# Kernel optimization log

Measured on AMD Instinct MI355X. Metric: run time of the kernel, lower is better.

The kernel has to match this reference:

```python
import jax, jax.numpy as jnp
import numpy as np

S = 8            # n_internal_streams
N = 2**S - 1     # 255 cliques (all non-empty subsets of streams)
D = 32           # half_dim = consciousness_dim // 2
INPUT_DIM = 512
NUM_ITER = 5
B = 1024


def _configs():
    # binary membership of each clique (non-empty subsets), [N, S]
    return ((np.arange(1, 2**S)[:, None] >> np.arange(S)) & 1).astype(np.float32)


def setup_inputs() -> dict:
    key = jax.random.key(0)
    ks = jax.random.split(key, 10)
    cfg = _configs()
    depths = cfg.sum(-1)
    # topological amplitude init: gaussian profile over clique depth
    center, sigma = S / 2.0, S / 3.0
    prof = np.exp(-((depths - center) ** 2) / (2 * sigma ** 2))
    prof = prof / (np.linalg.norm(prof) + 1e-8)
    psi_A0 = jnp.asarray(np.broadcast_to(prof[None, :, None], (1, N, D)).copy(),
                         jnp.float32) + jax.random.normal(ks[0], (1, N, D)) * 0.01
    inp = {
        'network_state': jax.random.normal(ks[1], (B, INPUT_DIM), jnp.float32),
        'W_streams': jax.random.normal(ks[2], (S * D, INPUT_DIM)) / np.sqrt(INPUT_DIM),
        'b_streams': jnp.zeros((S * D,), jnp.float32),
        'W_A': jax.random.normal(ks[3], (D, D)) / np.sqrt(D),
        'b_A': jnp.zeros((D,), jnp.float32),
        'W_phi': jax.random.normal(ks[4], (D, D)) / np.sqrt(D),
        'b_phi': jnp.zeros((D,), jnp.float32),
        'psi_A0': psi_A0,
        'psi_phi0': jax.random.normal(ks[5], (1, N, D)) * 0.3,
        'W_comp': jax.random.normal(ks[6], (32, N)) / np.sqrt(N),
        'b_comp': jnp.zeros((32,), jnp.float32),
        'W_read': jax.random.normal(ks[7], (2 * D, 32 * D)) / np.sqrt(32 * D),
        'b_read': jnp.zeros((2 * D,), jnp.float32),
        'alpha_kin': jnp.asarray(0.5, jnp.float32),
        'mass_sq': jnp.asarray(0.1, jnp.float32),
        'potential_weight': jnp.asarray(0.3, jnp.float32),
        'input_weight': jnp.asarray(0.5, jnp.float32),
        'evolution_rate': jnp.asarray(0.3, jnp.float32),
        'phase_coupling': jnp.asarray(1.0, jnp.float32),
    }
    return inp


def reference(network_state, W_streams, b_streams, W_A, b_A, W_phi, b_phi,
              psi_A0, psi_phi0, W_comp, b_comp, W_read, b_read,
              alpha_kin, mass_sq, potential_weight, input_weight,
              evolution_rate, phase_coupling):
    cfg = jnp.asarray(_configs())                      # [N,S]
    depths = cfg.sum(-1)                               # [N]
    # Hamming-distance kernel between clique configurations
    Ham = cfg @ (1.0 - cfg).T + (1.0 - cfg) @ cfg.T    # [N,N]
    K = jnp.exp(-Ham / S)
    krow = K.sum(1)                                    # [N]

    Bb = network_state.shape[0]
    feats = (network_state @ W_streams.T + b_streams).reshape(Bb, S, D)
    # clique features: mean of member-stream features
    cf = jnp.einsum('ns,bsd->bnd', cfg, feats) / depths[None, :, None]
    A_input = jax.nn.softplus(cf @ W_A.T + b_A)        # [B,N,D]
    phi_input = jnp.pi * jnp.tanh(cf @ W_phi.T + b_phi)

    A = jax.nn.softplus(jnp.broadcast_to(psi_A0, (Bb, N, D)))
    phi = jnp.broadcast_to(psi_phi0, (Bb, N, D))
    dt = jax.nn.sigmoid(evolution_rate)

    for _ in range(NUM_ITER):
        # laplacian: sum_j K_ij (A_j - A_i) / N  (factorized, same math)
        KA = jnp.einsum('ij,bjd->bid', K, A)
        lap = (KA - krow[None, :, None] * A) / N
        sp, cp = jnp.sin(phi), jnp.cos(phi)
        Ks = jnp.einsum('ij,bjd->bid', K, sp)
        Kc = jnp.einsum('ij,bjd->bid', K, cp)
        # sum_j K_ij A_i sin(phi_j - phi_i) / N
        pc = A * (cp * Ks - sp * Kc) / N
        # nonlocal potential: V_i = sum_j K_ij A_j cos(phi_j - phi_i) / N
        KAc = jnp.einsum('ij,bjd->bid', K, A * cp)
        KAs = jnp.einsum('ij,bjd->bid', K, A * sp)
        V = (cp * KAc + sp * KAs) / N
        input_drive = A_input * jnp.sin(phi_input - phi)
        dA = (alpha_kin * lap + potential_weight * V - mass_sq * A
              + input_weight * (A_input - A))
        A = jax.nn.softplus(A + dt * dA)               # updated A used in dphi
        dphi = alpha_kin * pc / (A + 1e-8) + input_weight * input_drive
        phi = phi + dt * dphi
        # per-clique norm clip to 1
        norms = jnp.maximum(jnp.linalg.norm(A, axis=-1, keepdims=True), 1e-8)
        A = A * jnp.where(norms > 1.0, 1.0 / norms, 1.0)

    A_t = jnp.swapaxes(A, 1, 2)                        # [B,D,N]
    Ac = jax.nn.relu(A_t @ W_comp.T + b_comp)          # [B,D,32]
    ro = Ac.reshape(Bb, -1) @ W_read.T + b_read        # [B,2D]
    amplitude = jax.nn.softplus(ro[:, :D])
    phase = jnp.tanh(ro[:, D:] * phase_coupling) * jnp.pi
    psi = (amplitude * jnp.cos(phase)).astype(jnp.complex64) + 1j * (amplitude * jnp.sin(phase)).astype(jnp.complex64)
    return psi, amplitude, phase
```

## Files before the change

kernel.cpp:

```cpp
#include <hip/hip_runtime.h>
#include <math.h>

#define PI_F   3.14159265358979f
#define QF     0.88249690258459546f
#define INV255 (1.0f/255.0f)

__device__ __forceinline__ float softplus_f(float x){
    return fmaxf(x, 0.0f) + __logf(1.0f + __expf(-fabsf(x)));
}
__device__ __forceinline__ float tanh_fast(float x){
    const float e = __expf(2.0f*x);
    return fmaf(-2.0f, __builtin_amdgcn_rcpf(e + 1.0f), 1.0f);
}

template<int CTRL>
__device__ __forceinline__ float dppmov(float x){
    return __int_as_float(__builtin_amdgcn_mov_dpp(__float_as_int(x), CTRL, 0xF, 0xF, false));
}
__device__ __forceinline__ float lxor1 (float x){ return dppmov<0xB1>(x);  }
__device__ __forceinline__ float lxor2 (float x){ return dppmov<0x4E>(x);  }
__device__ __forceinline__ float lxor8 (float x){ return dppmov<0x128>(x); }
__device__ __forceinline__ float lxor4 (float x){ return __int_as_float(__builtin_amdgcn_ds_swizzle(__float_as_int(x), 0x101F)); }
__device__ __forceinline__ float lxor16(float x){ return __int_as_float(__builtin_amdgcn_ds_swizzle(__float_as_int(x), 0x401F)); }
__device__ __forceinline__ float lxor32(float x){ return __shfl_xor(x, 32, 64); }

template<int CTRL>
__device__ __forceinline__ float dppadd(float v){
    return v + __int_as_float(__builtin_amdgcn_update_dpp(0, __float_as_int(v), CTRL, 0xF, 0xF, true));
}
__device__ __forceinline__ float wave_sum63(float v){
    v = dppadd<0x111>(v);
    v = dppadd<0x112>(v);
    v = dppadd<0x114>(v);
    v = dppadd<0x118>(v);
    v = dppadd<0x142>(v);
    v = dppadd<0x143>(v);
    return v;
}

template<int NA>
__device__ __forceinline__ void bflyN(float (&x)[NA][4]){
    const float qv = QF;
    #pragma unroll
    for (int a = 0; a < NA; a++){
        #pragma unroll
        for (int r = 0; r < 4; r++) x[a][r] = fmaf(lxor1 (x[a][r]), qv, x[a][r]);
    }
    #pragma unroll
    for (int a = 0; a < NA; a++){
        #pragma unroll
        for (int r = 0; r < 4; r++) x[a][r] = fmaf(lxor2 (x[a][r]), qv, x[a][r]);
    }
    #pragma unroll
    for (int a = 0; a < NA; a++){
        #pragma unroll
        for (int r = 0; r < 4; r++) x[a][r] = fmaf(lxor8 (x[a][r]), qv, x[a][r]);
    }
    #pragma unroll
    for (int a = 0; a < NA; a++){
        #pragma unroll
        for (int r = 0; r < 4; r++) x[a][r] = fmaf(lxor4 (x[a][r]), qv, x[a][r]);
    }
    #pragma unroll
    for (int a = 0; a < NA; a++){
        #pragma unroll
        for (int r = 0; r < 4; r++) x[a][r] = fmaf(lxor16(x[a][r]), qv, x[a][r]);
    }
    #pragma unroll
    for (int a = 0; a < NA; a++){
        #pragma unroll
        for (int r = 0; r < 4; r++) x[a][r] = fmaf(lxor32(x[a][r]), qv, x[a][r]);
    }
    #pragma unroll
    for (int a = 0; a < NA; a++){
        float t0 = x[a][0], t2 = x[a][2];
        x[a][0] = fmaf(QF, x[a][1], x[a][0]);
        x[a][1] = fmaf(QF, t0,      x[a][1]);
        x[a][2] = fmaf(QF, x[a][3], x[a][2]);
        x[a][3] = fmaf(QF, t2,      x[a][3]);
        t0 = x[a][0]; float t1 = x[a][1];
        x[a][0] = fmaf(QF, x[a][2], x[a][0]);
        x[a][1] = fmaf(QF, x[a][3], x[a][1]);
        x[a][2] = fmaf(QF, t0,      x[a][2]);
        x[a][3] = fmaf(QF, t1,      x[a][3]);
    }
}

__global__ __launch_bounds__(256) void prep_kernel(
        const float* __restrict__ Ws,    const float* __restrict__ psiA0,
        const float* __restrict__ psiP0, const float* __restrict__ p_alpha,
        const float* __restrict__ p_msq, const float* __restrict__ p_pw,
        const float* __restrict__ p_iw,  const float* __restrict__ p_evo,
        float* __restrict__ WsT,  float* __restrict__ Xc,  float* __restrict__ P0c,
        float* __restrict__ S0c,  float* __restrict__ C0c, float* __restrict__ F0c)
{
    if (blockIdx.x < 32){
        __shared__ float tile[64][65];
        const int rt = blockIdx.x & 3, ct = blockIdx.x >> 2;
        const int r0 = rt*64, c0t = ct*64;
        const int tx = threadIdx.x & 63, ty = threadIdx.x >> 6;
        #pragma unroll
        for (int k = 0; k < 16; k++){
            const int row = ty*16 + k;
            tile[row][tx] = Ws[(r0+row)*512 + c0t + tx];
        }
        __syncthreads();
        #pragma unroll
        for (int k = 0; k < 16; k++){
            const int row = ty*16 + k;
            WsT[(c0t+row)*256 + r0 + tx] = tile[tx][row];
        }
        return;
    }
    const int tid = threadIdx.x;
    const int w = tid >> 6, l = tid & 63;
    const float alpha = p_alpha[0], msq = p_msq[0], pw = p_pw[0], iw = p_iw[0];
    const float dt   = 1.0f / (1.0f + __expf(-p_evo[0]));
    const float dta  = dt * alpha * INV255;
    const float dtpw = dt * pw * INV255;
    const float c0   = 1.0f - dt * (msq + iw);
    const float m0 = (l == 0) ? 0.0f : 1.0f;
    int nn[4]; float krow[4];
    float c18;
    { const float t1 = 1.0f + QF, t2 = t1*t1, t4 = t2*t2; c18 = t4*t4; }
    #pragma unroll
    for (int r = 0; r < 4; r++){
        nn[r] = l + 64*r;
        krow[r] = c18 - __expf(-0.125f * (float)__popc(nn[r]));
    }
    #pragma unroll
    for (int dd = 0; dd < 8; dd++){
        const int d = w*8 + dd;
        float A0[4], ph0[4], sp[4], cp[4];
        float x[5][4];
        #pragma unroll
        for (int r = 0; r < 4; r++){
            const int n = nn[r];
            A0[r]  = (n > 0) ? softplus_f(psiA0[(n-1)*32 + d]) : 0.0f;
            ph0[r] = (n > 0) ? psiP0[(n-1)*32 + d] : 0.0f;
            sp[r] = __sinf(ph0[r]); cp[r] = __cosf(ph0[r]);
            const float mk = (r == 0) ? m0 : 1.0f;
            const float xa = A0[r] * mk;
            x[0][r] = xa;
            x[1][r] = sp[r] * mk;
            x[2][r] = cp[r] * mk;
            x[3][r] = xa * cp[r];
            x[4][r] = xa * sp[r];
        }
        bflyN<5>(x);
        #pragma unroll
        for (int r = 0; r < 4; r++){
            const float Ao   = A0[r];
            const float lapp = fmaf(-krow[r], Ao, x[0][r]);
            const float Vp   = fmaf(cp[r], x[3][r], sp[r]*x[4][r]);
            const float Pp   = fmaf(-sp[r], x[2][r], cp[r]*x[1][r]);
            float X = c0 * Ao;
            X = fmaf(dta,  lapp, X);
            X = fmaf(dtpw, Vp,   X);
            const int idx = d*256 + nn[r];
            Xc[idx]  = X;
            P0c[idx] = dta * Ao * Pp;
            S0c[idx] = sp[r];
            C0c[idx] = cp[r];
            F0c[idx] = ph0[r];
        }
    }
}

template<bool USET>
__global__ __launch_bounds__(256) void fused_kernel(
        const float* __restrict__ ns,
        const float* __restrict__ Ws,
        const float* __restrict__ WsT,
        const float* __restrict__ bs,
        const float* __restrict__ WA,
        const float* __restrict__ bA,
        const float* __restrict__ WP,
        const float* __restrict__ bP,
        const float* __restrict__ psiA0,
        const float* __restrict__ psiP0,
        const float* __restrict__ Xc,
        const float* __restrict__ P0c,
        const float* __restrict__ S0c,
        const float* __restrict__ C0c,
        const float* __restrict__ F0c,
        const float* __restrict__ Wcomp,
        const float* __restrict__ bcomp,
        const float* __restrict__ Wread,
        const float* __restrict__ bread,
        const float* __restrict__ p_alpha, const float* __restrict__ p_msq,
        const float* __restrict__ p_pw,    const float* __restrict__ p_iw,
        const float* __restrict__ p_evo,   const float* __restrict__ p_pcpl,
        float* __restrict__ out, int Bb)
{
    __shared__ __align__(16) float nsb[512];
    __shared__ __align__(16) float fe[256];
    __shared__ __align__(16) float hA[256];
    __shared__ __align__(16) float hP[256];
    __shared__ __align__(16) float red[2][1024];
    __shared__ __align__(16) float ac[1024];
    __shared__ __align__(16) float rop[256];

    const int b   = blockIdx.x;
    const int tid = threadIdx.x;
    const int w   = tid >> 6, l = tid & 63;

    const float alpha = p_alpha[0], msq = p_msq[0], pw = p_pw[0], iw = p_iw[0];
    const float pcpl  = p_pcpl[0];
    const float dt    = 1.0f / (1.0f + __expf(-p_evo[0]));
    const float dta  = dt * alpha * INV255;
    const float dtpw = dt * pw * INV255;
    const float c0   = 1.0f - dt * (msq + iw);
    const float dtiw = dt * iw;

    nsb[tid]       = ns[b*512 + tid];
    nsb[tid + 256] = ns[b*512 + 256 + tid];
    __syncthreads();
    if (USET){
        float f = bs[tid];
        const float4* nb4 = (const float4*)nsb;
        #pragma unroll 8
        for (int j4 = 0; j4 < 128; j4++){
            const float4 nv = nb4[j4];
            const float* col = WsT + j4*1024 + tid;
            f = fmaf(col[0],   nv.x, f);
            f = fmaf(col[256], nv.y, f);
            f = fmaf(col[512], nv.z, f);
            f = fmaf(col[768], nv.w, f);
        }
        fe[tid] = f;
    } else {
        float f = bs[tid];
        const float4* wr  = (const float4*)(Ws + tid*512);
        const float4* nb4 = (const float4*)nsb;
        #pragma unroll 8
        for (int i = 0; i < 128; i++){
            const float4 wv = wr[i], nv = nb4[i];
            f = fmaf(wv.x, nv.x, f); f = fmaf(wv.y, nv.y, f);
            f = fmaf(wv.z, nv.z, f); f = fmaf(wv.w, nv.w, f);
        }
        fe[tid] = f;
    }
    __syncthreads();
    {
        const int s = tid >> 5, d = tid & 31;
        float a = 0.0f, p = 0.0f;
        #pragma unroll 8
        for (int dp = 0; dp < 32; dp++){
            const float fv = fe[s*32 + dp];
            a = fmaf(WA[d*32 + dp], fv, a);
            p = fmaf(WP[d*32 + dp], fv, p);
        }
        hA[tid] = a; hP[tid] = p;
    }
    __syncthreads();

    int   nn[4];
    float krow[4], rdep[4];
    const float m0 = (l == 0) ? 0.0f : 1.0f;
    float c18;
    { const float t1 = 1.0f + QF, t2 = t1*t1, t4 = t2*t2; c18 = t4*t4; }
    #pragma unroll
    for (int r = 0; r < 4; r++){
        nn[r] = l + 64*r;
        const int pop = __popc(nn[r]);
        krow[r]  = c18 - __expf(-0.125f * (float)pop);
        rdep[r]  = 1.0f / (float)(pop ? pop : 1);
    }

    float A[8][4], phi[8][4], CAp[8][4], Dsp[8][4], Dcp[8][4];
    float nrm0[4] = {0.f, 0.f, 0.f, 0.f};

    #pragma unroll
    for (int dd = 0; dd < 8; dd++){
        const int d = w*8 + dd;
        const float bAd = bA[d], bPd = bP[d];
        float gA_[8], gP_[8];
        #pragma unroll
        for (int s = 0; s < 8; s++){ gA_[s] = hA[s*32 + d]; gP_[s] = hP[s*32 + d]; }
        #pragma unroll
        for (int r = 0; r < 4; r++){
            float sA = 0.0f, sP = 0.0f;
            #pragma unroll
            for (int s = 0; s < 8; s++){
                if ((nn[r] >> s) & 1){ sA += gA_[s]; sP += gP_[s]; }
            }
            const float uA  = fmaf(sA, rdep[r], bAd);
            const float uP  = fmaf(sP, rdep[r], bPd);
            const float Ain = softplus_f(uA);
            const float pin = PI_F * tanh_fast(uP);
            const float si = __sinf(pin), ci = __cosf(pin);
            const float ca = dtiw * Ain;
            CAp[dd][r] = ca; Dsp[dd][r] = ca * si; Dcp[dd][r] = ca * ci;
            if (USET){
                const int idx = d*256 + nn[r];
                const float An = softplus_f(Xc[idx] + ca);
                const float rr = __builtin_amdgcn_rcpf(An + 1e-8f);
                float pb = fmaf(Dsp[dd][r], C0c[idx], F0c[idx]);
                pb = fmaf(-Dcp[dd][r], S0c[idx], pb);
                phi[dd][r] = fmaf(P0c[idx], rr, pb);
                A[dd][r]   = An;
                nrm0[r]    = fmaf(An, An, nrm0[r]);
            } else {
                const int nm1 = (nn[r] > 0) ? (nn[r] - 1) : 0;
                A[dd][r]   = softplus_f(psiA0[nm1*32 + d]);
                phi[dd][r] = psiP0[nm1*32 + d];
            }
        }
    }

    if (USET){
        #pragma unroll
        for (int r = 0; r < 4; r++) red[0][w*256 + nn[r]] = nrm0[r];
        __syncthreads();
        float scl[4];
        #pragma unroll
        for (int r = 0; r < 4; r++){
            const float t = red[0][nn[r]] + red[0][256 + nn[r]]
                          + red[0][512 + nn[r]] + red[0][768 + nn[r]];
            scl[r] = (t > 1.0f) ? rsqrtf(t) : 1.0f;
        }
        #pragma unroll
        for (int dd = 0; dd < 8; dd++)
            #pragma unroll
            for (int r = 0; r < 4; r++) A[dd][r] *= scl[r];
    }

    const int NFULL = USET ? 3 : 4;
    for (int it = 0; it < NFULL; it++){
        const int pbuf = USET ? ((it + 1) & 1) : (it & 1);
        float nrm[4] = {0.f, 0.f, 0.f, 0.f};
        #pragma unroll
        for (int dd = 0; dd < 8; dd++){
            float sp[4], cp[4];
            float x[5][4];
            {
                sp[0] = __sinf(phi[dd][0]); cp[0] = __cosf(phi[dd][0]);
                const float xa = A[dd][0] * m0;
                x[0][0] = xa;
                x[1][0] = sp[0] * m0;
                x[2][0] = cp[0] * m0;
                x[3][0] = xa * cp[0];
                x[4][0] = xa * sp[0];
            }
            #pragma unroll
            for (int r = 1; r < 4; r++){
                sp[r] = __sinf(phi[dd][r]); cp[r] = __cosf(phi[dd][r]);
                const float xa = A[dd][r];
                x[0][r] = xa;
                x[1][r] = sp[r];
                x[2][r] = cp[r];
                x[3][r] = xa * cp[r];
                x[4][r] = xa * sp[r];
            }
            bflyN<5>(x);
            #pragma unroll
            for (int r = 0; r < 4; r++){
                const float Ao   = A[dd][r];
                const float lapp = fmaf(-krow[r], Ao, x[0][r]);
                const float Vp   = fmaf(cp[r], x[3][r], sp[r]*x[4][r]);
                float Aarg = fmaf(c0, Ao, CAp[dd][r]);
                Aarg = fmaf(dta,  lapp, Aarg);
                Aarg = fmaf(dtpw, Vp,   Aarg);
                const float An = softplus_f(Aarg);
                const float Pp = fmaf(-sp[r], x[2][r], cp[r]*x[1][r]);
                const float rr = __builtin_amdgcn_rcpf(An + 1e-8f);
                float pb = fmaf(Dsp[dd][r], cp[r], phi[dd][r]);
                pb = fmaf(-Dcp[dd][r], sp[r], pb);
                phi[dd][r] = fmaf(dta*Ao, Pp*rr, pb);
                A[dd][r]   = An;
                nrm[r]     = fmaf(An, An, nrm[r]);
            }
        }
        #pragma unroll
        for (int r = 0; r < 4; r++) red[pbuf][w*256 + nn[r]] = nrm[r];
        __syncthreads();
        float scl[4];
        #pragma unroll
        for (int r = 0; r < 4; r++){
            const float t = red[pbuf][nn[r]] + red[pbuf][256 + nn[r]]
                          + red[pbuf][512 + nn[r]] + red[pbuf][768 + nn[r]];
            scl[r] = (t > 1.0f) ? rsqrtf(t) : 1.0f;
        }
        #pragma unroll
        for (int dd = 0; dd < 8; dd++)
            #pragma unroll
            for (int r = 0; r < 4; r++) A[dd][r] *= scl[r];
    }

    {
        float nrm[4] = {0.f, 0.f, 0.f, 0.f};
        #pragma unroll
        for (int dd = 0; dd < 8; dd++){
            float sp[4], cp[4];
            float y[3][4];
            {
                sp[0] = __sinf(phi[dd][0]); cp[0] = __cosf(phi[dd][0]);
                const float xa = A[dd][0] * m0;
                y[0][0] = xa;
                y[1][0] = xa * cp[0];
                y[2][0] = xa * sp[0];
            }
            #pragma unroll
            for (int r = 1; r < 4; r++){
                sp[r] = __sinf(phi[dd][r]); cp[r] = __cosf(phi[dd][r]);
                const float xa = A[dd][r];
                y[0][r] = xa;
                y[1][r] = xa * cp[r];
                y[2][r] = xa * sp[r];
            }
            bflyN<3>(y);
            #pragma unroll
            for (int r = 0; r < 4; r++){
                const float Ao   = A[dd][r];
                const float lapp = fmaf(-krow[r], Ao, y[0][r]);
                const float Vp   = fmaf(cp[r], y[1][r], sp[r]*y[2][r]);
                float Aarg = fmaf(c0, Ao, CAp[dd][r]);
                Aarg = fmaf(dta,  lapp, Aarg);
                Aarg = fmaf(dtpw, Vp,   Aarg);
                const float An = softplus_f(Aarg);
                A[dd][r]   = An;
                nrm[r]     = fmaf(An, An, nrm[r]);
            }
        }
        #pragma unroll
        for (int r = 0; r < 4; r++) red[0][w*256 + nn[r]] = nrm[r];
        __syncthreads();
        float scl[4];
        #pragma unroll
        for (int r = 0; r < 4; r++){
            const float t = red[0][nn[r]] + red[0][256 + nn[r]]
                          + red[0][512 + nn[r]] + red[0][768 + nn[r]];
            scl[r] = (t > 1.0f) ? rsqrtf(t) : 1.0f;
        }
        #pragma unroll
        for (int dd = 0; dd < 8; dd++)
            #pragma unroll
            for (int r = 0; r < 4; r++) A[dd][r] *= scl[r];
    }

    #pragma unroll
    for (int dd = 0; dd < 8; dd++) A[dd][0] *= m0;

    for (int c = 0; c < 32; c++){
        float wv[4];
        #pragma unroll
        for (int r = 0; r < 4; r++){
            const int idx = c*255 + nn[r] - 1;
            wv[r] = Wcomp[idx < 0 ? 0 : idx];
        }
        const float bc = bcomp[c];
        #pragma unroll
        for (int dd = 0; dd < 8; dd++){
            float v = wv[0] * A[dd][0];
            v = fmaf(wv[1], A[dd][1], v);
            v = fmaf(wv[2], A[dd][2], v);
            v = fmaf(wv[3], A[dd][3], v);
            v = wave_sum63(v);
            if (l == 63)
                ac[(w*8 + dd)*32 + c] = fmaxf(v + bc, 0.0f);
        }
    }
    __syncthreads();

    {
        const int k = tid >> 2, part = tid & 3;
        const float4* Wr4 = (const float4*)Wread + k*256;
        const float4* ac4 = (const float4*)ac;
        float s = 0.0f;
        #pragma unroll 4
        for (int jj = 0; jj < 64; jj++){
            const int j4 = part + 4*jj;
            const float4 wv = Wr4[j4];
            const float4 av = ac4[j4];
            s = fmaf(wv.x, av.x, s); s = fmaf(wv.y, av.y, s);
            s = fmaf(wv.z, av.z, s); s = fmaf(wv.w, av.w, s);
        }
        rop[tid] = s;
    }
    __syncthreads();
    if (tid < 32){
        const float ra = rop[tid*4] + rop[tid*4+1] + rop[tid*4+2] + rop[tid*4+3] + bread[tid];
        const int   t2 = tid + 32;
        const float rp = rop[t2*4] + rop[t2*4+1] + rop[t2*4+2] + rop[t2*4+3] + bread[t2];
        const float amp = softplus_f(ra);
        const float ph  = PI_F * tanhf(rp * pcpl);
        const float cph = __cosf(ph);
        const int o = b*32 + tid;
        out[o]         = amp * cph;
        out[Bb*32 + o] = amp;
        out[Bb*64 + o] = ph;
    }
}

extern "C" void kernel_launch(void* const* d_in, const int* in_sizes, int n_in,
                              void* d_out, int out_size, void* d_ws, size_t ws_size,
                              hipStream_t stream) {
    const float* ns      = (const float*)d_in[0];
    const float* Ws      = (const float*)d_in[1];
    const float* bs      = (const float*)d_in[2];
    const float* WA      = (const float*)d_in[3];
    const float* bA      = (const float*)d_in[4];
    const float* WP      = (const float*)d_in[5];
    const float* bP      = (const float*)d_in[6];
    const float* psiA0   = (const float*)d_in[7];
    const float* psiP0   = (const float*)d_in[8];
    const float* Wcomp   = (const float*)d_in[9];
    const float* bcomp   = (const float*)d_in[10];
    const float* Wread   = (const float*)d_in[11];
    const float* bread   = (const float*)d_in[12];
    const float* p_alpha = (const float*)d_in[13];
    const float* p_msq   = (const float*)d_in[14];
    const float* p_pw    = (const float*)d_in[15];
    const float* p_iw    = (const float*)d_in[16];
    const float* p_evo   = (const float*)d_in[17];
    const float* p_pcpl  = (const float*)d_in[18];

    const int Bb = in_sizes[0] / 512;

    const size_t need = (size_t)(512*256 + 5*32*256) * sizeof(float);
    if (ws_size >= need){
        float* WsT = (float*)d_ws;
        float* Xc  = WsT + 512*256;
        float* P0c = Xc  + 32*256;
        float* S0c = P0c + 32*256;
        float* C0c = S0c + 32*256;
        float* F0c = C0c + 32*256;
        prep_kernel<<<33, 256, 0, stream>>>(Ws, psiA0, psiP0,
                                            p_alpha, p_msq, p_pw, p_iw, p_evo,
                                            WsT, Xc, P0c, S0c, C0c, F0c);
        fused_kernel<true><<<Bb, 256, 0, stream>>>(ns, Ws, WsT, bs, WA, bA, WP, bP,
                                                   psiA0, psiP0, Xc, P0c, S0c, C0c, F0c,
                                                   Wcomp, bcomp, Wread, bread,
                                                   p_alpha, p_msq, p_pw, p_iw,
                                                   p_evo, p_pcpl, (float*)d_out, Bb);
    } else {
        fused_kernel<false><<<Bb, 256, 0, stream>>>(ns, Ws, nullptr, bs, WA, bA, WP, bP,
                                                    psiA0, psiP0,
                                                    nullptr, nullptr, nullptr, nullptr, nullptr,
                                                    Wcomp, bcomp, Wread, bread,
                                                    p_alpha, p_msq, p_pw, p_iw,
                                                    p_evo, p_pcpl, (float*)d_out, Bb);
    }
}
```

Measured before the change: 313.0 us.

## Double block size to 512 threads, halving per-thread D slices and register state

Launches 512 threads per batch element instead of 256. Each of the eight waves now owns four D channels instead of eight, which halves the per-thread register arrays. Every stage is re-split to match: the stream projection uses a two-way K split with an LDS reduction, WA and WP are handled by separate thread halves, norm reductions sum eight partials, and the readout uses an eight-way split. The aim is lower register pressure, so more waves can be resident and latency is better hidden. The cost is more shared memory and extra reduction work per block.

```diff
diff --git a/kernel.cpp b/kernel.cpp
--- a/kernel.cpp
+++ b/kernel.cpp
@@ -168,7 +168,7 @@
 }
 
 template<bool USET>
-__global__ __launch_bounds__(256) void fused_kernel(
+__global__ __launch_bounds__(512, 4) void fused_kernel(
         const float* __restrict__ ns,
         const float* __restrict__ Ws,
         const float* __restrict__ WsT,
@@ -197,9 +197,9 @@
     __shared__ __align__(16) float fe[256];
     __shared__ __align__(16) float hA[256];
     __shared__ __align__(16) float hP[256];
-    __shared__ __align__(16) float red[2][1024];
+    __shared__ __align__(16) float red[2][2048];
     __shared__ __align__(16) float ac[1024];
-    __shared__ __align__(16) float rop[256];
+    __shared__ __align__(16) float rop[512];
 
     const int b   = blockIdx.x;
     const int tid = threadIdx.x;
@@ -213,80 +213,82 @@
     const float c0   = 1.0f - dt * (msq + iw);
     const float dtiw = dt * iw;
 
-    nsb[tid]       = ns[b*512 + tid];
-    nsb[tid + 256] = ns[b*512 + 256 + tid];
-    __syncthreads();
-    if (USET){
-        float f = bs[tid];
-        const float4* nb4 = (const float4*)nsb;
-        #pragma unroll 8
-        for (int j4 = 0; j4 < 128; j4++){
-            const float4 nv = nb4[j4];
-            const float* col = WsT + j4*1024 + tid;
-            f = fmaf(col[0],   nv.x, f);
-            f = fmaf(col[256], nv.y, f);
-            f = fmaf(col[512], nv.z, f);
-            f = fmaf(col[768], nv.w, f);
-        }
-        fe[tid] = f;
-    } else {
-        float f = bs[tid];
-        const float4* wr  = (const float4*)(Ws + tid*512);
-        const float4* nb4 = (const float4*)nsb;
-        #pragma unroll 8
-        for (int i = 0; i < 128; i++){
-            const float4 wv = wr[i], nv = nb4[i];
-            f = fmaf(wv.x, nv.x, f); f = fmaf(wv.y, nv.y, f);
-            f = fmaf(wv.z, nv.z, f); f = fmaf(wv.w, nv.w, f);
-        }
-        fe[tid] = f;
-    }
+    nsb[tid] = ns[b*512 + tid];
     __syncthreads();
     {
-        const int s = tid >> 5, d = tid & 31;
-        float a = 0.0f, p = 0.0f;
+        const int k = tid >> 1, part = tid & 1;
+        float f = (part == 0) ? bs[k] : 0.0f;
+        if (USET){
+            const float4* nb4 = (const float4*)nsb + part*64;
+            const float*  colb = WsT + (part*64)*1024 + k;
+            #pragma unroll 8
+            for (int j4 = 0; j4 < 64; j4++){
+                const float4 nv = nb4[j4];
+                const float* col = colb + j4*1024;
+                f = fmaf(col[0],   nv.x, f);
+                f = fmaf(col[256], nv.y, f);
+                f = fmaf(col[512], nv.z, f);
+                f = fmaf(col[768], nv.w, f);
+            }
+        } else {
+            const float4* wr  = (const float4*)(Ws + k*512) + part*64;
+            const float4* nb4 = (const float4*)nsb + part*64;
+            #pragma unroll 8
+            for (int i = 0; i < 64; i++){
+                const float4 wv = wr[i], nv = nb4[i];
+                f = fmaf(wv.x, nv.x, f); f = fmaf(wv.y, nv.y, f);
+                f = fmaf(wv.z, nv.z, f); f = fmaf(wv.w, nv.w, f);
+            }
+        }
+        red[0][part*256 + k] = f;
+    }
+    __syncthreads();
+    if (tid < 256) fe[tid] = red[0][tid] + red[0][256 + tid];
+    __syncthreads();
+    {
+        const int t2 = tid & 255;
+        const int s = t2 >> 5, d2 = t2 & 31;
+        const float* Wm = (tid < 256) ? WA : WP;
+        float acc = 0.0f;
         #pragma unroll 8
-        for (int dp = 0; dp < 32; dp++){
-            const float fv = fe[s*32 + dp];
-            a = fmaf(WA[d*32 + dp], fv, a);
-            p = fmaf(WP[d*32 + dp], fv, p);
-        }
-        hA[tid] = a; hP[tid] = p;
+        for (int dp = 0; dp < 32; dp++)
+            acc = fmaf(Wm[d2*32 + dp], fe[s*32 + dp], acc);
+        if (tid < 256) hA[t2] = acc; else hP[t2] = acc;
     }
     __syncthreads();
 
     int   nn[4];
-    float krow[4], rdep[4];
+    float krow[4];
     const float m0 = (l == 0) ? 0.0f : 1.0f;
     float c18;
     { const float t1 = 1.0f + QF, t2 = t1*t1, t4 = t2*t2; c18 = t4*t4; }
     #pragma unroll
     for (int r = 0; r < 4; r++){
         nn[r] = l + 64*r;
-        const int pop = __popc(nn[r]);
-        krow[r]  = c18 - __expf(-0.125f * (float)pop);
-        rdep[r]  = 1.0f / (float)(pop ? pop : 1);
-    }
-
-    float A[8][4], phi[8][4], CAp[8][4], Dsp[8][4], Dcp[8][4];
+        krow[r] = c18 - __expf(-0.125f * (float)__popc(nn[r]));
+    }
+
+    float A[4][4], phi[4][4], CAp[4][4], Dsp[4][4], Dcp[4][4];
     float nrm0[4] = {0.f, 0.f, 0.f, 0.f};
 
     #pragma unroll
-    for (int dd = 0; dd < 8; dd++){
-        const int d = w*8 + dd;
+    for (int dd = 0; dd < 4; dd++){
+        const int d = w*4 + dd;
         const float bAd = bA[d], bPd = bP[d];
         float gA_[8], gP_[8];
         #pragma unroll
         for (int s = 0; s < 8; s++){ gA_[s] = hA[s*32 + d]; gP_[s] = hP[s*32 + d]; }
         #pragma unroll
         for (int r = 0; r < 4; r++){
+            const int pop = __popc(nn[r]);
+            const float rdep = 1.0f / (float)(pop ? pop : 1);
             float sA = 0.0f, sP = 0.0f;
             #pragma unroll
             for (int s = 0; s < 8; s++){
                 if ((nn[r] >> s) & 1){ sA += gA_[s]; sP += gP_[s]; }
             }
-            const float uA  = fmaf(sA, rdep[r], bAd);
-            const float uP  = fmaf(sP, rdep[r], bPd);
+            const float uA  = fmaf(sA, rdep, bAd);
+            const float uP  = fmaf(sP, rdep, bPd);
             const float Ain = softplus_f(uA);
             const float pin = PI_F * tanh_fast(uP);
             const float si = __sinf(pin), ci = __cosf(pin);
@@ -316,12 +318,13 @@
         float scl[4];
         #pragma unroll
         for (int r = 0; r < 4; r++){
-            const float t = red[0][nn[r]] + red[0][256 + nn[r]]
-                          + red[0][512 + nn[r]] + red[0][768 + nn[r]];
+            const int n = nn[r];
+            const float t = red[0][n]        + red[0][256 + n]  + red[0][512 + n]  + red[0][768 + n]
+                          + red[0][1024 + n] + red[0][1280 + n] + red[0][1536 + n] + red[0][1792 + n];
             scl[r] = (t > 1.0f) ? rsqrtf(t) : 1.0f;
         }
         #pragma unroll
-        for (int dd = 0; dd < 8; dd++)
+        for (int dd = 0; dd < 4; dd++)
             #pragma unroll
             for (int r = 0; r < 4; r++) A[dd][r] *= scl[r];
     }
@@ -331,7 +334,7 @@
         const int pbuf = USET ? ((it + 1) & 1) : (it & 1);
         float nrm[4] = {0.f, 0.f, 0.f, 0.f};
         #pragma unroll
-        for (int dd = 0; dd < 8; dd++){
+        for (int dd = 0; dd < 4; dd++){
             float sp[4], cp[4];
             float x[5][4];
             {
@@ -378,12 +381,13 @@
         float scl[4];
         #pragma unroll
         for (int r = 0; r < 4; r++){
-            const float t = red[pbuf][nn[r]] + red[pbuf][256 + nn[r]]
-                          + red[pbuf][512 + nn[r]] + red[pbuf][768 + nn[r]];
+            const int n = nn[r];
+            const float t = red[pbuf][n]        + red[pbuf][256 + n]  + red[pbuf][512 + n]  + red[pbuf][768 + n]
+                          + red[pbuf][1024 + n] + red[pbuf][1280 + n] + red[pbuf][1536 + n] + red[pbuf][1792 + n];
             scl[r] = (t > 1.0f) ? rsqrtf(t) : 1.0f;
         }
         #pragma unroll
-        for (int dd = 0; dd < 8; dd++)
+        for (int dd = 0; dd < 4; dd++)
             #pragma unroll
             for (int r = 0; r < 4; r++) A[dd][r] *= scl[r];
     }
@@ -391,7 +395,7 @@
     {
         float nrm[4] = {0.f, 0.f, 0.f, 0.f};
         #pragma unroll
-        for (int dd = 0; dd < 8; dd++){
+        for (int dd = 0; dd < 4; dd++){
             float sp[4], cp[4];
             float y[3][4];
             {
@@ -429,18 +433,19 @@
         float scl[4];
         #pragma unroll
         for (int r = 0; r < 4; r++){
-            const float t = red[0][nn[r]] + red[0][256 + nn[r]]
-                          + red[0][512 + nn[r]] + red[0][768 + nn[r]];
+            const int n = nn[r];
+            const float t = red[0][n]        + red[0][256 + n]  + red[0][512 + n]  + red[0][768 + n]
+                          + red[0][1024 + n] + red[0][1280 + n] + red[0][1536 + n] + red[0][1792 + n];
             scl[r] = (t > 1.0f) ? rsqrtf(t) : 1.0f;
         }
         #pragma unroll
-        for (int dd = 0; dd < 8; dd++)
+        for (int dd = 0; dd < 4; dd++)
             #pragma unroll
             for (int r = 0; r < 4; r++) A[dd][r] *= scl[r];
     }
 
     #pragma unroll
-    for (int dd = 0; dd < 8; dd++) A[dd][0] *= m0;
+    for (int dd = 0; dd < 4; dd++) A[dd][0] *= m0;
 
     for (int c = 0; c < 32; c++){
         float wv[4];
@@ -451,26 +456,26 @@
         }
         const float bc = bcomp[c];
         #pragma unroll
-        for (int dd = 0; dd < 8; dd++){
+        for (int dd = 0; dd < 4; dd++){
             float v = wv[0] * A[dd][0];
             v = fmaf(wv[1], A[dd][1], v);
             v = fmaf(wv[2], A[dd][2], v);
             v = fmaf(wv[3], A[dd][3], v);
             v = wave_sum63(v);
             if (l == 63)
-                ac[(w*8 + dd)*32 + c] = fmaxf(v + bc, 0.0f);
+                ac[(w*4 + dd)*32 + c] = fmaxf(v + bc, 0.0f);
         }
     }
     __syncthreads();
 
     {
-        const int k = tid >> 2, part = tid & 3;
+        const int k = tid >> 3, part = tid & 7;
         const float4* Wr4 = (const float4*)Wread + k*256;
         const float4* ac4 = (const float4*)ac;
         float s = 0.0f;
         #pragma unroll 4
-        for (int jj = 0; jj < 64; jj++){
-            const int j4 = part + 4*jj;
+        for (int jj = 0; jj < 32; jj++){
+            const int j4 = part + 8*jj;
             const float4 wv = Wr4[j4];
             const float4 av = ac4[j4];
             s = fmaf(wv.x, av.x, s); s = fmaf(wv.y, av.y, s);
@@ -480,9 +485,12 @@
     }
     __syncthreads();
     if (tid < 32){
-        const float ra = rop[tid*4] + rop[tid*4+1] + rop[tid*4+2] + rop[tid*4+3] + bread[tid];
-        const int   t2 = tid + 32;
-        const float rp = rop[t2*4] + rop[t2*4+1] + rop[t2*4+2] + rop[t2*4+3] + bread[t2];
+        float ra = bread[tid], rp = bread[tid + 32];
+        #pragma unroll
+        for (int p = 0; p < 8; p++){
+            ra += rop[tid*8 + p];
+            rp += rop[(tid + 32)*8 + p];
+        }
         const float amp = softplus_f(ra);
         const float ph  = PI_F * tanhf(rp * pcpl);
         const float cph = __cosf(ph);
@@ -529,13 +537,13 @@
         prep_kernel<<<33, 256, 0, stream>>>(Ws, psiA0, psiP0,
                                             p_alpha, p_msq, p_pw, p_iw, p_evo,
                                             WsT, Xc, P0c, S0c, C0c, F0c);
-        fused_kernel<true><<<Bb, 256, 0, stream>>>(ns, Ws, WsT, bs, WA, bA, WP, bP,
+        fused_kernel<true><<<Bb, 512, 0, stream>>>(ns, Ws, WsT, bs, WA, bA, WP, bP,
                                                    psiA0, psiP0, Xc, P0c, S0c, C0c, F0c,
                                                    Wcomp, bcomp, Wread, bread,
                                                    p_alpha, p_msq, p_pw, p_iw,
                                                    p_evo, p_pcpl, (float*)d_out, Bb);
     } else {
-        fused_kernel<false><<<Bb, 256, 0, stream>>>(ns, Ws, nullptr, bs, WA, bA, WP, bP,
+        fused_kernel<false><<<Bb, 512, 0, stream>>>(ns, Ws, nullptr, bs, WA, bA, WP, bP,
                                                     psiA0, psiP0,
                                                     nullptr, nullptr, nullptr, nullptr, nullptr,
                                                     Wcomp, bcomp, Wread, bread,
```

New measurement: 314.3 us. About the same (+0.4%).
